# Kernel optimization log

Hardware: AMD Instinct MI355X
Metric: run time of the kernel (lower is better)

## Reference

```python
import jax, jax.numpy as jnp
import numpy as np


def setup_inputs() -> dict:
    key = jax.random.key(0)
    kq, kk, kv = jax.random.split(key, 3)
    B, S, D = 8, 4096, 64
    q = jax.random.normal(kq, (B, S, D), dtype=jnp.float32)
    k = jax.random.normal(kk, (B, S, D), dtype=jnp.float32)
    v = jax.random.normal(kv, (B, S, D), dtype=jnp.float32)
    mask = jnp.ones((B, S), dtype=jnp.float32)
    return {"q": q, "k": k, "v": v, "mask": mask}


def reference(q, k, v, mask):
    # scores: [B, Sq, Sk], scaled by sqrt(D)
    scale = 1.0 / jnp.sqrt(jnp.asarray(q.shape[-1], q.dtype))
    w = jnp.einsum("bqd,bkd->bqk", q, k) * scale
    # softmax over dim=2 (keys axis for rank-3 input)
    w = jax.nn.softmax(w, axis=2)
    x = jnp.einsum("bqk,bkd->bqd", w, v)
    # post-hoc multiplicative mask on outputs
    x = x * mask[..., None]
    return x
```

## Files before the change

kernel.cpp:

```cpp
#include <hip/hip_runtime.h>

typedef __attribute__((ext_vector_type(8))) short short8;
typedef __attribute__((ext_vector_type(4))) short short4v;
typedef __attribute__((ext_vector_type(4))) float floatx4;
typedef __attribute__((ext_vector_type(4))) unsigned short ushortx4;
typedef __attribute__((ext_vector_type(8))) unsigned short ushortx8;
typedef unsigned int u32;
typedef __attribute__((ext_vector_type(2))) u32 u32x2;
typedef __attribute__((ext_vector_type(4))) u32 u32x4;

#define MFMA_K32(A, B, C) __builtin_amdgcn_mfma_f32_16x16x32_bf16(A, B, C, 0, 0, 0)

#if __has_builtin(__builtin_amdgcn_mfma_f32_16x16x16bf16_1k)
#define HAVE_K16 1
#define MFMA_K16(A, B, C) __builtin_amdgcn_mfma_f32_16x16x16bf16_1k(A, B, C, 0, 0, 0)
#else
#define HAVE_K16 0
#endif

#if __has_builtin(__builtin_amdgcn_exp2f)
#define EXP2(x) __builtin_amdgcn_exp2f(x)
#else
#define EXP2(x) exp2f(x)
#endif

__device__ __forceinline__ unsigned short f2bf(float f) {
  u32 u = __builtin_bit_cast(u32, f);
  u += 0x7FFFu + ((u >> 16) & 1u);
  return (unsigned short)(u >> 16);
}
__device__ __forceinline__ void load_lds16(const void* g, void* l) {
  __builtin_amdgcn_global_load_lds((const __attribute__((address_space(1))) u32*)g,
                                   (__attribute__((address_space(3))) u32*)l, 16, 0, 0);
}

__global__ __launch_bounds__(256) void prep_kv(
    const float* __restrict__ k, const float* __restrict__ v,
    unsigned short* __restrict__ kb, unsigned short* __restrict__ vt) {
  __shared__ float tileT[64 * 68];
  int blk = blockIdx.x;
  int t = threadIdx.x;
  if (blk < 512) {
    size_t base = (size_t)blk * 4096 + t * 4;
#pragma unroll
    for (int i = 0; i < 4; i++) {
      size_t off = base + (size_t)i * 1024;
      floatx4 f = *(const floatx4*)(k + off);
      ushortx4 h;
      h[0] = f2bf(f[0]); h[1] = f2bf(f[1]); h[2] = f2bf(f[2]); h[3] = f2bf(f[3]);
      *(ushortx4*)(kb + off) = h;
    }
  } else {
    blk -= 512;
    const int b = blk >> 6, si = blk & 63;
    const int r = t >> 2, c4 = (t & 3) * 16;
    const float* vp = v + ((size_t)b * 4096 + si * 64 + r) * 64 + c4;
#pragma unroll
    for (int i = 0; i < 4; i++) {
      floatx4 f = *(const floatx4*)(vp + i * 4);
#pragma unroll
      for (int j = 0; j < 4; j++) tileT[(c4 + i * 4 + j) * 68 + r] = f[j];
    }
    __syncthreads();
    unsigned short* vo = vt + ((size_t)b * 64 + si) * 4096;
#pragma unroll
    for (int i = 0; i < 2; i++) {
      const int u = t + i * 256;
      const int d = u >> 3, p = u & 7;
      const int s = p ^ (d & 7);
      const float* src = tileT + d * 68 + s * 8;
      floatx4 f0 = *(const floatx4*)src;
      floatx4 f1 = *(const floatx4*)(src + 4);
      ushortx8 h;
#pragma unroll
      for (int j = 0; j < 4; j++) { h[j] = f2bf(f0[j]); h[4 + j] = f2bf(f1[j]); }
      *(ushortx8*)(vo + d * 64 + p * 8) = h;
    }
  }
}

__global__ __launch_bounds__(256, 3) void attn(
    const float* __restrict__ q, const unsigned short* __restrict__ kb,
    const unsigned short* __restrict__ vt, const float* __restrict__ mask,
    float* __restrict__ out) {
  __shared__ __align__(16) char smem_raw[37888];
  unsigned short* smem = (unsigned short*)smem_raw;
  const int tid = threadIdx.x;
  const int wave = tid >> 6, lane = tid & 63;
  const int c = lane & 15, quad = lane >> 4;
  const int b = blockIdx.x & 7, qt = blockIdx.x >> 3;
  const int q0 = qt * 64;

  const unsigned short* kB = kb + (size_t)b * (4096 * 64);
  const unsigned short* vtB = vt + (size_t)b * (64 * 4096);

  const float qscale = 0.18033688011112042f;
  short8 qf[4][2];
#pragma unroll
  for (int nt = 0; nt < 4; nt++)
#pragma unroll
    for (int kc = 0; kc < 2; kc++) {
      const float* qp = q + ((size_t)b * 4096 + q0 + nt * 16 + c) * 64 + kc * 32 + quad * 8;
      floatx4 f0 = *(const floatx4*)qp;
      floatx4 f1 = *(const floatx4*)(qp + 4);
      short8 s;
#pragma unroll
      for (int j = 0; j < 4; j++) {
        s[j] = (short)f2bf(f0[j] * qscale);
        s[4 + j] = (short)f2bf(f1[j] * qscale);
      }
      qf[nt][kc] = s;
    }

  floatx4 o[4][4];
#pragma unroll
  for (int mt = 0; mt < 4; mt++)
#pragma unroll
    for (int nt = 0; nt < 4; nt++) o[mt][nt] = (floatx4){0.f, 0.f, 0.f, 0.f};
  float llane[4] = {0.f, 0.f, 0.f, 0.f};

  const int r8 = lane >> 3, cs8 = lane & 7;
  const int cl7 = c & 7;

  auto stage = [&](int t, int buf) {
    unsigned short* dK = smem + buf * 8192;
    unsigned short* dV = dK + 4096;
    const unsigned short* gK = kB + (size_t)(t * 64) * 64;
    const unsigned short* gV = vtB + (size_t)t * 4096;
#pragma unroll
    for (int j = 0; j < 2; j++) {
      const int i = wave * 2 + j;
      load_lds16(gK + (i * 8 + r8) * 64 + (cs8 ^ r8) * 8, dK + i * 512);
      load_lds16(gV + i * 512 + lane * 8, dV + i * 512);
    }
  };

  stage(0, 0);
  __syncthreads();

  for (int t = 0; t < 64; t++) {
    if (t + 1 < 64) stage(t + 1, (t + 1) & 1);

    const unsigned short* K = smem + (t & 1) * 8192;
    const unsigned short* Vt = K + 4096;

    short8 kf[2];
#pragma unroll
    for (int kc = 0; kc < 2; kc++)
      kf[kc] = *(const short8*)(K + (wave * 16 + c) * 64 + ((kc * 4 + quad) ^ cl7) * 8);

    u32x2 vv[4];
#pragma unroll
    for (int mt = 0; mt < 4; mt++) {
      const int phys = (2 * wave + (quad >> 1)) ^ cl7;
      vv[mt] = *(const u32x2*)(Vt + (mt * 16 + c) * 64 + phys * 8 + (quad & 1) * 4);
    }

#pragma unroll
    for (int nt = 0; nt < 4; nt++) {
      floatx4 s = (floatx4){0.f, 0.f, 0.f, 0.f};
      s = MFMA_K32(kf[0], qf[nt][0], s);
      s = MFMA_K32(kf[1], qf[nt][1], s);
      u32 u0 = __builtin_bit_cast(u32, EXP2(s[0]));
      u32 u1 = __builtin_bit_cast(u32, EXP2(s[1]));
      u32 u2 = __builtin_bit_cast(u32, EXP2(s[2]));
      u32 u3 = __builtin_bit_cast(u32, EXP2(s[3]));
      llane[nt] += __builtin_bit_cast(float, u0 & 0xFFFF0000u) +
                   __builtin_bit_cast(float, u1 & 0xFFFF0000u) +
                   __builtin_bit_cast(float, u2 & 0xFFFF0000u) +
                   __builtin_bit_cast(float, u3 & 0xFFFF0000u);
      u32 plo = __builtin_amdgcn_perm(u1, u0, 0x07060302u);
      u32 phi = __builtin_amdgcn_perm(u3, u2, 0x07060302u);
#if HAVE_K16
      short4v pf = __builtin_bit_cast(short4v, (u32x2){plo, phi});
#pragma unroll
      for (int mt = 0; mt < 4; mt++) {
        short4v va = __builtin_bit_cast(short4v, vv[mt]);
        o[mt][nt] = MFMA_K16(va, pf, o[mt][nt]);
      }
#else
      short8 pf = __builtin_bit_cast(short8, (u32x4){plo, phi, 0u, 0u});
#pragma unroll
      for (int mt = 0; mt < 4; mt++) {
        short8 va = __builtin_bit_cast(short8, (u32x4){vv[mt][0], vv[mt][1], 0u, 0u});
        o[mt][nt] = MFMA_K32(va, pf, o[mt][nt]);
      }
#endif
    }

    __syncthreads();
  }

#pragma unroll
  for (int nt = 0; nt < 4; nt++) {
    llane[nt] += __shfl_xor(llane[nt], 16, 64);
    llane[nt] += __shfl_xor(llane[nt], 32, 64);
  }

  float* obuf = (float*)smem_raw;
  float* lbuf = obuf + 9216;
  if (lane < 16) {
#pragma unroll
    for (int nt = 0; nt < 4; nt++) lbuf[wave * 64 + nt * 16 + c] = llane[nt];
  }
  if (wave < 2) {
    float* ob = obuf + wave * 4608;
#pragma unroll
    for (int mt = 0; mt < 4; mt++)
#pragma unroll
      for (int nt = 0; nt < 4; nt++)
        *(floatx4*)(ob + (nt * 16 + c) * 72 + mt * 16 + quad * 4) = o[mt][nt];
  }
  __syncthreads();
  if (wave >= 2) {
    float* ob = obuf + (wave - 2) * 4608;
#pragma unroll
    for (int mt = 0; mt < 4; mt++)
#pragma unroll
      for (int nt = 0; nt < 4; nt++) {
        float* a = ob + (nt * 16 + c) * 72 + mt * 16 + quad * 4;
        floatx4 cur = *(floatx4*)a;
        *(floatx4*)a = cur + o[mt][nt];
      }
  }
  __syncthreads();

  const int row = tid >> 2, dg = (tid & 3) * 16;
  const float l = lbuf[row] + lbuf[64 + row] + lbuf[128 + row] + lbuf[192 + row];
  const float sc = mask[b * 4096 + q0 + row] / l;
  float* op = out + ((size_t)b * 4096 + q0 + row) * 64 + dg;
#pragma unroll
  for (int i = 0; i < 4; i++) {
    floatx4 a = *(const floatx4*)(obuf + row * 72 + dg + i * 4);
    floatx4 b2 = *(const floatx4*)(obuf + 4608 + row * 72 + dg + i * 4);
    *(floatx4*)(op + i * 4) = (a + b2) * sc;
  }
}

extern "C" void kernel_launch(void* const* d_in, const int* in_sizes, int n_in,
                              void* d_out, int out_size, void* d_ws, size_t ws_size,
                              hipStream_t stream) {
  const float* q = (const float*)d_in[0];
  const float* k = (const float*)d_in[1];
  const float* v = (const float*)d_in[2];
  const float* mask = (const float*)d_in[3];
  unsigned short* kb = (unsigned short*)d_ws;
  unsigned short* vt = kb + 8 * 4096 * 64;
  prep_kv<<<1024, 256, 0, stream>>>(k, v, kb, vt);
  attn<<<512, 256, 0, stream>>>(q, kb, vt, mask, (float*)d_out);
}
```

Baseline: 127.9 us.

## Give each wave private LDS K/V slices to drop per-tile block barriers

Each wave now stages only its own 16-key K rows and matching V^T columns into a private double-buffered LDS region. It waits on its own vmcnt instead of a block-wide __syncthreads every tile. The softmax denominator is computed by an extra MFMA against a ones vector rather than by scalar adds and shuffles. prep_kv is merged into 512 blocks that each do both the K conversion and the V transpose, with the V swizzle removed. Occupancy hint drops to 2 blocks per CU. The risks are the hardcoded waitcnt encodings and lost occupancy.

Result: faster. 124.5 us (-2.6%).

```diff
diff --git a/kernel.cpp b/kernel.cpp
--- a/kernel.cpp
+++ b/kernel.cpp
@@ -24,6 +24,9 @@
 #define EXP2(x) exp2f(x)
 #endif
 
+#define WAIT_VM4() __builtin_amdgcn_s_waitcnt(0x0F74)
+#define WAIT_VM0() __builtin_amdgcn_s_waitcnt(0x0F70)
+
 __device__ __forceinline__ unsigned short f2bf(float f) {
   u32 u = __builtin_bit_cast(u32, f);
   u += 0x7FFFu + ((u >> 16) & 1u);
@@ -38,48 +41,41 @@
     const float* __restrict__ k, const float* __restrict__ v,
     unsigned short* __restrict__ kb, unsigned short* __restrict__ vt) {
   __shared__ float tileT[64 * 68];
-  int blk = blockIdx.x;
-  int t = threadIdx.x;
-  if (blk < 512) {
-    size_t base = (size_t)blk * 4096 + t * 4;
-#pragma unroll
-    for (int i = 0; i < 4; i++) {
-      size_t off = base + (size_t)i * 1024;
-      floatx4 f = *(const floatx4*)(k + off);
-      ushortx4 h;
-      h[0] = f2bf(f[0]); h[1] = f2bf(f[1]); h[2] = f2bf(f[2]); h[3] = f2bf(f[3]);
-      *(ushortx4*)(kb + off) = h;
-    }
-  } else {
-    blk -= 512;
-    const int b = blk >> 6, si = blk & 63;
-    const int r = t >> 2, c4 = (t & 3) * 16;
-    const float* vp = v + ((size_t)b * 4096 + si * 64 + r) * 64 + c4;
-#pragma unroll
-    for (int i = 0; i < 4; i++) {
-      floatx4 f = *(const floatx4*)(vp + i * 4);
-#pragma unroll
-      for (int j = 0; j < 4; j++) tileT[(c4 + i * 4 + j) * 68 + r] = f[j];
-    }
-    __syncthreads();
-    unsigned short* vo = vt + ((size_t)b * 64 + si) * 4096;
-#pragma unroll
-    for (int i = 0; i < 2; i++) {
-      const int u = t + i * 256;
-      const int d = u >> 3, p = u & 7;
-      const int s = p ^ (d & 7);
-      const float* src = tileT + d * 68 + s * 8;
-      floatx4 f0 = *(const floatx4*)src;
-      floatx4 f1 = *(const floatx4*)(src + 4);
-      ushortx8 h;
-#pragma unroll
-      for (int j = 0; j < 4; j++) { h[j] = f2bf(f0[j]); h[4 + j] = f2bf(f1[j]); }
-      *(ushortx8*)(vo + d * 64 + p * 8) = h;
-    }
-  }
-}
-
-__global__ __launch_bounds__(256, 3) void attn(
+  const int blk = blockIdx.x, tid = threadIdx.x;
+  size_t base = (size_t)blk * 4096 + tid * 4;
+#pragma unroll
+  for (int i = 0; i < 4; i++) {
+    size_t off = base + (size_t)i * 1024;
+    floatx4 f = *(const floatx4*)(k + off);
+    ushortx4 h;
+    h[0] = f2bf(f[0]); h[1] = f2bf(f[1]); h[2] = f2bf(f[2]); h[3] = f2bf(f[3]);
+    *(ushortx4*)(kb + off) = h;
+  }
+  const int r = tid >> 2, c4 = (tid & 3) * 16;
+  const float* vp = v + ((size_t)blk * 64 + r) * 64 + c4;
+#pragma unroll
+  for (int i = 0; i < 4; i++) {
+    floatx4 f = *(const floatx4*)(vp + i * 4);
+#pragma unroll
+    for (int j = 0; j < 4; j++) tileT[(c4 + i * 4 + j) * 68 + r] = f[j];
+  }
+  __syncthreads();
+  unsigned short* vo = vt + (size_t)blk * 4096;
+#pragma unroll
+  for (int i = 0; i < 2; i++) {
+    const int u = tid + i * 256;
+    const int d = u >> 3, p = u & 7;
+    const float* src = tileT + d * 68 + p * 8;
+    floatx4 f0 = *(const floatx4*)src;
+    floatx4 f1 = *(const floatx4*)(src + 4);
+    ushortx8 h;
+#pragma unroll
+    for (int j = 0; j < 4; j++) { h[j] = f2bf(f0[j]); h[4 + j] = f2bf(f1[j]); }
+    *(ushortx8*)(vo + d * 64 + p * 8) = h;
+  }
+}
+
+__global__ __launch_bounds__(256, 2) void attn(
     const float* __restrict__ q, const unsigned short* __restrict__ kb,
     const unsigned short* __restrict__ vt, const float* __restrict__ mask,
     float* __restrict__ out) {
@@ -112,49 +108,61 @@
       qf[nt][kc] = s;
     }
 
-  floatx4 o[4][4];
+  floatx4 o[4][4], o_l[4];
 #pragma unroll
   for (int mt = 0; mt < 4; mt++)
 #pragma unroll
     for (int nt = 0; nt < 4; nt++) o[mt][nt] = (floatx4){0.f, 0.f, 0.f, 0.f};
-  float llane[4] = {0.f, 0.f, 0.f, 0.f};
+#pragma unroll
+  for (int nt = 0; nt < 4; nt++) o_l[nt] = (floatx4){0.f, 0.f, 0.f, 0.f};
+
+#if HAVE_K16
+  short4v ones_a;
+#pragma unroll
+  for (int j = 0; j < 4; j++) ones_a[j] = (short)0x3F80;
+#else
+  short8 ones_a;
+#pragma unroll
+  for (int j = 0; j < 8; j++) ones_a[j] = (short)0x3F80;
+#endif
 
   const int r8 = lane >> 3, cs8 = lane & 7;
-  const int cl7 = c & 7;
+  unsigned short* wbase = smem + wave * 4096;
+  const unsigned short* gK0 = kB + (size_t)(wave * 16 + r8) * 64 + (cs8 ^ r8) * 8;
+  const unsigned short* gV0 = vtB + (size_t)(lane >> 1) * 64 + wave * 16 + (lane & 1) * 8;
 
   auto stage = [&](int t, int buf) {
-    unsigned short* dK = smem + buf * 8192;
-    unsigned short* dV = dK + 4096;
-    const unsigned short* gK = kB + (size_t)(t * 64) * 64;
-    const unsigned short* gV = vtB + (size_t)t * 4096;
-#pragma unroll
-    for (int j = 0; j < 2; j++) {
-      const int i = wave * 2 + j;
-      load_lds16(gK + (i * 8 + r8) * 64 + (cs8 ^ r8) * 8, dK + i * 512);
-      load_lds16(gV + i * 512 + lane * 8, dV + i * 512);
+    unsigned short* Kd = wbase + buf * 2048;
+    const unsigned short* gk = gK0 + (size_t)t * 4096;
+    const unsigned short* gv = gV0 + (size_t)t * 4096;
+    load_lds16(gk, Kd);
+    load_lds16(gk + 8 * 64, Kd + 512);
+    load_lds16(gv, Kd + 1024);
+    load_lds16(gv + 32 * 64, Kd + 1536);
+  };
+
+  stage(0, 0);
+
+  for (int t = 0; t < 64; t++) {
+    if (t < 63) {
+      stage(t + 1, (t + 1) & 1);
+      WAIT_VM4();
+    } else {
+      WAIT_VM0();
     }
-  };
-
-  stage(0, 0);
-  __syncthreads();
-
-  for (int t = 0; t < 64; t++) {
-    if (t + 1 < 64) stage(t + 1, (t + 1) & 1);
-
-    const unsigned short* K = smem + (t & 1) * 8192;
-    const unsigned short* Vt = K + 4096;
+    __builtin_amdgcn_sched_barrier(0);
+
+    const unsigned short* Kb = wbase + (t & 1) * 2048;
+    const unsigned short* Vb = Kb + 1024;
 
     short8 kf[2];
 #pragma unroll
     for (int kc = 0; kc < 2; kc++)
-      kf[kc] = *(const short8*)(K + (wave * 16 + c) * 64 + ((kc * 4 + quad) ^ cl7) * 8);
-
+      kf[kc] = *(const short8*)(Kb + c * 64 + ((kc * 4 + quad) ^ (c & 7)) * 8);
     u32x2 vv[4];
 #pragma unroll
-    for (int mt = 0; mt < 4; mt++) {
-      const int phys = (2 * wave + (quad >> 1)) ^ cl7;
-      vv[mt] = *(const u32x2*)(Vt + (mt * 16 + c) * 64 + phys * 8 + (quad & 1) * 4);
-    }
+    for (int mt = 0; mt < 4; mt++)
+      vv[mt] = *(const u32x2*)(Vb + (mt * 16 + c) * 16 + quad * 4);
 
 #pragma unroll
     for (int nt = 0; nt < 4; nt++) {
@@ -165,19 +173,14 @@
       u32 u1 = __builtin_bit_cast(u32, EXP2(s[1]));
       u32 u2 = __builtin_bit_cast(u32, EXP2(s[2]));
       u32 u3 = __builtin_bit_cast(u32, EXP2(s[3]));
-      llane[nt] += __builtin_bit_cast(float, u0 & 0xFFFF0000u) +
-                   __builtin_bit_cast(float, u1 & 0xFFFF0000u) +
-                   __builtin_bit_cast(float, u2 & 0xFFFF0000u) +
-                   __builtin_bit_cast(float, u3 & 0xFFFF0000u);
       u32 plo = __builtin_amdgcn_perm(u1, u0, 0x07060302u);
       u32 phi = __builtin_amdgcn_perm(u3, u2, 0x07060302u);
 #if HAVE_K16
       short4v pf = __builtin_bit_cast(short4v, (u32x2){plo, phi});
 #pragma unroll
-      for (int mt = 0; mt < 4; mt++) {
-        short4v va = __builtin_bit_cast(short4v, vv[mt]);
-        o[mt][nt] = MFMA_K16(va, pf, o[mt][nt]);
-      }
+      for (int mt = 0; mt < 4; mt++)
+        o[mt][nt] = MFMA_K16(__builtin_bit_cast(short4v, vv[mt]), pf, o[mt][nt]);
+      o_l[nt] = MFMA_K16(ones_a, pf, o_l[nt]);
 #else
       short8 pf = __builtin_bit_cast(short8, (u32x4){plo, phi, 0u, 0u});
 #pragma unroll
@@ -185,23 +188,17 @@
         short8 va = __builtin_bit_cast(short8, (u32x4){vv[mt][0], vv[mt][1], 0u, 0u});
         o[mt][nt] = MFMA_K32(va, pf, o[mt][nt]);
       }
+      o_l[nt] = MFMA_K32(ones_a, pf, o_l[nt]);
 #endif
     }
-
-    __syncthreads();
-  }
-
-#pragma unroll
-  for (int nt = 0; nt < 4; nt++) {
-    llane[nt] += __shfl_xor(llane[nt], 16, 64);
-    llane[nt] += __shfl_xor(llane[nt], 32, 64);
-  }
-
+  }
+
+  __syncthreads();
   float* obuf = (float*)smem_raw;
   float* lbuf = obuf + 9216;
   if (lane < 16) {
 #pragma unroll
-    for (int nt = 0; nt < 4; nt++) lbuf[wave * 64 + nt * 16 + c] = llane[nt];
+    for (int nt = 0; nt < 4; nt++) lbuf[wave * 64 + nt * 16 + c] = o_l[nt][0];
   }
   if (wave < 2) {
     float* ob = obuf + wave * 4608;
@@ -246,6 +243,6 @@
   const float* mask = (const float*)d_in[3];
   unsigned short* kb = (unsigned short*)d_ws;
   unsigned short* vt = kb + 8 * 4096 * 64;
-  prep_kv<<<1024, 256, 0, stream>>>(k, v, kb, vt);
+  prep_kv<<<512, 256, 0, stream>>>(k, v, kb, vt);
   attn<<<512, 256, 0, stream>>>(q, kb, vt, mask, (float*)d_out);
 }
```
